# Optimization experiments

Hardware: AMD Instinct MI355X
Metric: run time of the kernel (lower is better)

The kernel has to match this reference:

```python
import jax, jax.numpy as jnp
import numpy as np

KSIZE, H, W = 11, 256, 256
IN_C, OUT_C, B = 3, 64, 4


def _foveated_coords(height, width, k):
    """Integer foveated sampling coords [H, W, k, k] for y and x.

    Ring scale per kernel tap: Chebyshev dist from center -> 1/3/5/7.
    Matches FoveatedSamplingConv2d._create_all_foveated_kernels, where
    coords are exact integers, so bilinear grid_sample == integer gather.
    """
    c = k // 2
    ki = np.arange(k)
    dist = np.maximum(np.abs(ki[:, None] - c), np.abs(ki[None, :] - c))  # [k,k]
    scale = np.where(dist <= 1, 1, np.where(dist == 2, 3, np.where(dist == 3, 5, 7)))
    off_y = (ki[:, None] - c) * scale  # [k,k]
    off_x = (ki[None, :] - c) * scale  # [k,k]
    yy = np.arange(height)[:, None, None, None]
    xx = np.arange(width)[None, :, None, None]
    sy = np.clip(yy + off_y[None, None], 0, height - 1)  # [H,W,k,k]
    sx = np.clip(xx + off_x[None, None], 0, width - 1)   # [H,W,k,k]
    return jnp.asarray(sy, jnp.int32), jnp.asarray(sx, jnp.int32)


def setup_inputs() -> dict:
    key = jax.random.key(0)
    k1, k2, k3 = jax.random.split(key, 3)
    x = jax.random.normal(k1, (B, IN_C, H, W), dtype=jnp.float32)
    # Kaiming-uniform-ish init scale (exact distribution irrelevant for correctness)
    fan_in = IN_C * KSIZE * KSIZE
    bound = 1.0 / np.sqrt(fan_in)
    weight = jax.random.uniform(k2, (OUT_C, IN_C, KSIZE, KSIZE), dtype=jnp.float32,
                                minval=-bound, maxval=bound)
    bias = jax.random.uniform(k3, (OUT_C,), dtype=jnp.float32, minval=-bound, maxval=bound)
    sy, sx = _foveated_coords(H, W, KSIZE)
    return {"x": x, "weight": weight, "bias": bias, "sy": sy, "sx": sx}


def reference(x, weight, bias, sy, sx):
    # Irregular gather: sampled[b,c,h,w,ki,kj] = x[b,c, sy[h,w,ki,kj], sx[h,w,ki,kj]]
    sampled = x[:, :, sy, sx]  # [B, C, H, W, k, k]
    out = jnp.einsum('bchwkl,ockl->bohw', sampled, weight)
    return out + bias[None, :, None, None]
```

## Files before the change

### kernel.cpp

```cpp
#include <hip/hip_runtime.h>


#define HH 256
#define WW 256
#define INC 3
#define OC 64
#define KS 11
#define BB 4
#define NKC 12
#define PH 326
#define PW 512
#define PAD 35
#define NPAR 4
#define HALFR 163

typedef __attribute__((ext_vector_type(4))) float f32x4;
typedef __attribute__((ext_vector_type(8))) short s16x8;
typedef unsigned int u32;
typedef unsigned short u16;

static __device__ __forceinline__ u16 f2bf(float f) {
    u32 u = __builtin_bit_cast(u32, f);
    u32 r = (u + 0x7FFFu + ((u >> 16) & 1u)) >> 16;
    return (u16)r;
}

__global__ void __launch_bounds__(256)
prep_fused(const float* __restrict__ x, const float* __restrict__ w,
           u16* __restrict__ xs, u16* __restrict__ wf) {
    const int tid = threadIdx.x;
    if (blockIdx.x < 96) {
        int i = blockIdx.x * 256 + tid;
        int j    = i & 7;
        int lane = (i >> 3) & 63;
        int ot   = (i >> 9) & 3;
        int kc   = i >> 11;
        int o  = ot * 16 + (lane & 15);
        int k  = kc * 32 + ((lane >> 4) << 3) + j;
        int c  = k >> 7;
        int tt = k & 127;
        float val = 0.f;
        if (tt < 121) {
            int ky = tt / 11, kx = tt % 11;
            val = w[((o * INC + c) * KS + ky) * KS + kx];
        }
        wf[i] = f2bf(val);
    } else {
        const int pb = blockIdx.x - 96;
        const int k  = pb & 7;
        const int i  = pb >> 3;
        const int r  = i * 2 + (tid >> 7);
        const int zl = r / HALFR;
        const int pz = r - zl * HALFR;
        const int b    = k >> 1;
        const int py   = (k & 1) * HALFR + pz;
        const int c    = zl % INC;
        const int par  = zl / INC;
        const int z    = (b * NPAR + par) * INC + c;
        const int px0  = (tid & 127) * 4;
        const int sy   = min(max(py - PAD, 0), HH - 1);
        const float* src = x + (((size_t)b * INC + c) * HH + sy) * WW;
        ushort4 o4;
        int s0 = min(max(px0 + 0 - PAD + par, 0), WW - 1);
        int s1 = min(max(px0 + 1 - PAD + par, 0), WW - 1);
        int s2 = min(max(px0 + 2 - PAD + par, 0), WW - 1);
        int s3 = min(max(px0 + 3 - PAD + par, 0), WW - 1);
        o4.x = f2bf(src[s0]); o4.y = f2bf(src[s1]);
        o4.z = f2bf(src[s2]); o4.w = f2bf(src[s3]);
        *(ushort4*)&xs[((size_t)z * PH + py) * PW + px0] = o4;
    }
}

__global__ void __launch_bounds__(256, 3)
fov_mfma5(const u16* __restrict__ xs, const u16* __restrict__ wf,
          const float* __restrict__ bias, float* __restrict__ out) {
    __shared__ u32 offF[NKC * 32];
    const int tid = threadIdx.x;
    for (int t = tid; t < NKC * 32; t += 256) {
        int c = t >> 7, tt = t & 127;
        int dy = 0, dx = 0;
        if (tt < 121) {
            int ky = tt / 11, kx = tt - (tt / 11) * 11;
            int ay = ky - 5, ax = kx - 5;
            int d = max(abs(ay), abs(ax));
            int sc = (d <= 1) ? 1 : (d == 2 ? 3 : (d == 3 ? 5 : 7));
            dy = ay * sc; dx = ax * sc;
        }
        int par = (PAD + dx) & 3;
        offF[t] = (u32)(((((par * INC + c) * PH) + (PAD + dy)) * PW
                         + (PAD + dx - par)) * 2);
    }
    __syncthreads();

    const int lane = tid & 63;
    const int wv   = tid >> 6;
    const int obid = (blockIdx.x & 7) * 128 + (blockIdx.x >> 3);
    const int b = obid >> 8;
    const int h = obid & 255;
    const int g16 = lane & 15;
    const int kg  = lane >> 4;

    const char* xpb = (const char*)(xs + (size_t)b * (NPAR * INC * PH * PW));
    const u32 pxoff = (u32)((h * PW + wv * 64 + 4 * g16) * 2);
    const s16x8* wbase = (const s16x8*)wf;

    f32x4 acc[4][4];
#pragma unroll
    for (int T = 0; T < 4; ++T)
#pragma unroll
        for (int ob = 0; ob < 4; ++ob) acc[T][ob] = (f32x4){0, 0, 0, 0};

    uint2 G[3][8];
    s16x8 A[2][4];

#define STAGE_G(S, KC)                                                    \
    {                                                                     \
        const uint4* fp = (const uint4*)&offF[(KC) * 32 + kg * 8];        \
        const uint4 fA = fp[0], fB = fp[1];                               \
        G[S][0] = *(const uint2*)(xpb + (pxoff + fA.x));                  \
        G[S][1] = *(const uint2*)(xpb + (pxoff + fA.y));                  \
        G[S][2] = *(const uint2*)(xpb + (pxoff + fA.z));                  \
        G[S][3] = *(const uint2*)(xpb + (pxoff + fA.w));                  \
        G[S][4] = *(const uint2*)(xpb + (pxoff + fB.x));                  \
        G[S][5] = *(const uint2*)(xpb + (pxoff + fB.y));                  \
        G[S][6] = *(const uint2*)(xpb + (pxoff + fB.z));                  \
        G[S][7] = *(const uint2*)(xpb + (pxoff + fB.w));                  \
    }

    STAGE_G(0, 0)
    STAGE_G(1, 1)
    {
        const s16x8* wp = wbase + lane;
        A[0][0] = wp[0]; A[0][1] = wp[64]; A[0][2] = wp[128]; A[0][3] = wp[192];
    }

#pragma unroll
    for (int kc = 0; kc < NKC; ++kc) {
        const int cur = kc % 3;
        const int pre = (kc + 2) % 3;
        if (kc + 2 < NKC) STAGE_G(pre, kc + 2)
        if (kc + 1 < NKC) {
            const s16x8* wp = wbase + (((kc + 1) << 8) + lane);
            A[(kc + 1) & 1][0] = wp[0];   A[(kc + 1) & 1][1] = wp[64];
            A[(kc + 1) & 1][2] = wp[128]; A[(kc + 1) & 1][3] = wp[192];
        }
        __builtin_amdgcn_s_setprio(1);
#pragma unroll
        for (int T = 0; T < 4; ++T) {
            const u32 sel = (T & 1) ? 0x07060302u : 0x05040100u;
            const bool hi = (T >> 1) != 0;
            union { u32 u[4]; s16x8 v; } bu;
            bu.u[0] = __builtin_amdgcn_perm(hi ? G[cur][1].y : G[cur][1].x,
                                            hi ? G[cur][0].y : G[cur][0].x, sel);
            bu.u[1] = __builtin_amdgcn_perm(hi ? G[cur][3].y : G[cur][3].x,
                                            hi ? G[cur][2].y : G[cur][2].x, sel);
            bu.u[2] = __builtin_amdgcn_perm(hi ? G[cur][5].y : G[cur][5].x,
                                            hi ? G[cur][4].y : G[cur][4].x, sel);
            bu.u[3] = __builtin_amdgcn_perm(hi ? G[cur][7].y : G[cur][7].x,
                                            hi ? G[cur][6].y : G[cur][6].x, sel);

            acc[T][0] = __builtin_amdgcn_mfma_f32_16x16x32_bf16(A[kc & 1][0], bu.v, acc[T][0], 0, 0, 0);
            acc[T][1] = __builtin_amdgcn_mfma_f32_16x16x32_bf16(A[kc & 1][1], bu.v, acc[T][1], 0, 0, 0);
            acc[T][2] = __builtin_amdgcn_mfma_f32_16x16x32_bf16(A[kc & 1][2], bu.v, acc[T][2], 0, 0, 0);
            acc[T][3] = __builtin_amdgcn_mfma_f32_16x16x32_bf16(A[kc & 1][3], bu.v, acc[T][3], 0, 0, 0);
        }
        __builtin_amdgcn_s_setprio(0);
    }
#undef STAGE_G

    const int orow = kg << 2;
    const float4* bp = (const float4*)bias;
#pragma unroll
    for (int ob = 0; ob < 4; ++ob) {
        const float4 bb = bp[ob * 4 + kg];
        const float bv[4] = {bb.x, bb.y, bb.z, bb.w};
#pragma unroll
        for (int r = 0; r < 4; ++r) {
            const int o = ob * 16 + orow + r;
            f32x4 st;
            st[0] = acc[0][ob][r] + bv[r];
            st[1] = acc[1][ob][r] + bv[r];
            st[2] = acc[2][ob][r] + bv[r];
            st[3] = acc[3][ob][r] + bv[r];
            float* op = out + (((size_t)b * OC + o) * HH + h) * WW + wv * 64 + 4 * g16;
            __builtin_nontemporal_store(st, (f32x4*)op);
        }
    }
}

__global__ void fovconv_transpose_w(const float* __restrict__ w,
                                    float* __restrict__ wT) {
    int i = blockIdx.x * 256 + threadIdx.x;
    const int N = OC * INC * KS * KS;
    if (i < N) {
        int o  = i / (INC * KS * KS);
        int ct = i % (INC * KS * KS);
        wT[ct * OC + o] = w[i];
    }
}

__global__ void __launch_bounds__(256)
fovconv_main(const float* __restrict__ x, const float* __restrict__ wT,
             const float* __restrict__ bias, float* __restrict__ out) {
    const int wpix = threadIdx.x;
    const int h    = blockIdx.x & (HH - 1);
    const int b    = blockIdx.x >> 8;
    float acc[OC];
#pragma unroll
    for (int o = 0; o < OC; ++o) acc[o] = 0.f;
    const float* xbp = x + (size_t)b * INC * HH * WW;
    for (int k = 0; k < KS; ++k) {
        const int dy = k - 5;
        for (int l = 0; l < KS; ++l) {
            const int dx = l - 5;
            const int d  = max(abs(dy), abs(dx));
            const int scale = (d <= 1) ? 1 : (d == 2 ? 3 : (d == 3 ? 5 : 7));
            const int sy = min(max(h + dy * scale, 0), HH - 1);
            const int sx = min(max(wpix + dx * scale, 0), WW - 1);
            const int base = sy * WW + sx;
            const int t = k * KS + l;
#pragma unroll
            for (int c = 0; c < INC; ++c) {
                const float xv = xbp[c * (HH * WW) + base];
                const float* wp = wT + (c * (KS * KS) + t) * OC;
#pragma unroll
                for (int o = 0; o < OC; ++o)
                    acc[o] = fmaf(xv, wp[o], acc[o]);
            }
        }
    }
    float* op = out + (((size_t)b * OC) * HH + h) * WW + wpix;
#pragma unroll
    for (int o = 0; o < OC; ++o)
        op[(size_t)o * HH * WW] = acc[o] + bias[o];
}

extern "C" void kernel_launch(void* const* d_in, const int* in_sizes, int n_in,
                              void* d_out, int out_size, void* d_ws, size_t ws_size,
                              hipStream_t stream) {
    const float* x    = (const float*)d_in[0];
    const float* wgt  = (const float*)d_in[1];
    const float* bias = (const float*)d_in[2];
    float* out = (float*)d_out;

    const size_t xs_bytes = (size_t)BB * NPAR * INC * PH * PW * 2;
    const size_t wf_bytes = (size_t)NKC * 4 * 64 * 8 * 2;

    if (ws_size >= xs_bytes + wf_bytes) {
        u16* xsb = (u16*)d_ws;
        u16* wf  = (u16*)((char*)d_ws + xs_bytes);
        prep_fused<<<96 + 978 * 8, 256, 0, stream>>>(x, wgt, xsb, wf);
        fov_mfma5<<<BB * HH, 256, 0, stream>>>(xsb, wf, bias, out);
    } else {
        float* wT = (float*)d_ws;
        const int NW = OC * INC * KS * KS;
        fovconv_transpose_w<<<(NW + 255) / 256, 256, 0, stream>>>(wgt, wT);
        fovconv_main<<<BB * HH, 256, 0, stream>>>(x, wT, bias, out);
    }
}
```

Before: 36.65 us.

## Stage weights into LDS via direct global-to-LDS loads, shrink gather prefetch depth

Each block now copies the full bf16 weight fragment array (48KB) into shared memory at kernel start using global_load_lds, and reads A operands from LDS every k-chunk instead of prefetching them from global memory into registers. The gather pipeline is reduced from three stages to two, freeing registers. The intent is to cut per-wave global weight traffic and register pressure. The cost is a large LDS footprint, which may limit occupancy below the 3 blocks per CU requested in the launch bounds, plus a shallower latency-hiding window for the gathers.

```diff
diff --git a/kernel.cpp b/kernel.cpp
--- a/kernel.cpp
+++ b/kernel.cpp
@@ -74,8 +74,13 @@
 __global__ void __launch_bounds__(256, 3)
 fov_mfma5(const u16* __restrict__ xs, const u16* __restrict__ wf,
           const float* __restrict__ bias, float* __restrict__ out) {
+    __shared__ __align__(16) u32 swf[NKC * 1024];
     __shared__ u32 offF[NKC * 32];
-    const int tid = threadIdx.x;
+
+    const int tid  = threadIdx.x;
+    const int lane = tid & 63;
+    const int wv   = tid >> 6;
+
     for (int t = tid; t < NKC * 32; t += 256) {
         int c = t >> 7, tt = t & 127;
         int dy = 0, dx = 0;
@@ -90,10 +95,22 @@
         offF[t] = (u32)(((((par * INC + c) * PH) + (PAD + dy)) * PW
                          + (PAD + dx - par)) * 2);
     }
+
+    {
+        const char* wsrc = (const char*)wf;
+#pragma unroll
+        for (int j = 0; j < NKC; ++j) {
+            const int chunkbase = j * 256 + wv * 64;
+            __builtin_amdgcn_global_load_lds(
+                (const __attribute__((address_space(1))) void*)
+                    (wsrc + ((size_t)(chunkbase + lane) << 4)),
+                (__attribute__((address_space(3))) void*)
+                    ((char*)swf + ((size_t)chunkbase << 4)),
+                16, 0, 0);
+        }
+    }
     __syncthreads();
 
-    const int lane = tid & 63;
-    const int wv   = tid >> 6;
     const int obid = (blockIdx.x & 7) * 128 + (blockIdx.x >> 3);
     const int b = obid >> 8;
     const int h = obid & 255;
@@ -102,7 +119,7 @@
 
     const char* xpb = (const char*)(xs + (size_t)b * (NPAR * INC * PH * PW));
     const u32 pxoff = (u32)((h * PW + wv * 64 + 4 * g16) * 2);
-    const s16x8* wbase = (const s16x8*)wf;
+    const s16x8* wlds = (const s16x8*)swf;
 
     f32x4 acc[4][4];
 #pragma unroll
@@ -110,8 +127,7 @@
 #pragma unroll
         for (int ob = 0; ob < 4; ++ob) acc[T][ob] = (f32x4){0, 0, 0, 0};
 
-    uint2 G[3][8];
-    s16x8 A[2][4];
+    uint2 G[2][8];
 
 #define STAGE_G(S, KC)                                                    \
     {                                                                     \
@@ -128,22 +144,17 @@
     }
 
     STAGE_G(0, 0)
-    STAGE_G(1, 1)
-    {
-        const s16x8* wp = wbase + lane;
-        A[0][0] = wp[0]; A[0][1] = wp[64]; A[0][2] = wp[128]; A[0][3] = wp[192];
-    }
 
 #pragma unroll
     for (int kc = 0; kc < NKC; ++kc) {
-        const int cur = kc % 3;
-        const int pre = (kc + 2) % 3;
-        if (kc + 2 < NKC) STAGE_G(pre, kc + 2)
-        if (kc + 1 < NKC) {
-            const s16x8* wp = wbase + (((kc + 1) << 8) + lane);
-            A[(kc + 1) & 1][0] = wp[0];   A[(kc + 1) & 1][1] = wp[64];
-            A[(kc + 1) & 1][2] = wp[128]; A[(kc + 1) & 1][3] = wp[192];
-        }
+        const int cur = kc & 1;
+        if (kc + 1 < NKC) STAGE_G(cur ^ 1, kc + 1)
+
+        const s16x8 a0 = wlds[(kc << 8) + lane];
+        const s16x8 a1 = wlds[(kc << 8) + 64 + lane];
+        const s16x8 a2 = wlds[(kc << 8) + 128 + lane];
+        const s16x8 a3 = wlds[(kc << 8) + 192 + lane];
+
         __builtin_amdgcn_s_setprio(1);
 #pragma unroll
         for (int T = 0; T < 4; ++T) {
@@ -159,10 +170,10 @@
             bu.u[3] = __builtin_amdgcn_perm(hi ? G[cur][7].y : G[cur][7].x,
                                             hi ? G[cur][6].y : G[cur][6].x, sel);
 
-            acc[T][0] = __builtin_amdgcn_mfma_f32_16x16x32_bf16(A[kc & 1][0], bu.v, acc[T][0], 0, 0, 0);
-            acc[T][1] = __builtin_amdgcn_mfma_f32_16x16x32_bf16(A[kc & 1][1], bu.v, acc[T][1], 0, 0, 0);
-            acc[T][2] = __builtin_amdgcn_mfma_f32_16x16x32_bf16(A[kc & 1][2], bu.v, acc[T][2], 0, 0, 0);
-            acc[T][3] = __builtin_amdgcn_mfma_f32_16x16x32_bf16(A[kc & 1][3], bu.v, acc[T][3], 0, 0, 0);
+            acc[T][0] = __builtin_amdgcn_mfma_f32_16x16x32_bf16(a0, bu.v, acc[T][0], 0, 0, 0);
+            acc[T][1] = __builtin_amdgcn_mfma_f32_16x16x32_bf16(a1, bu.v, acc[T][1], 0, 0, 0);
+            acc[T][2] = __builtin_amdgcn_mfma_f32_16x16x32_bf16(a2, bu.v, acc[T][2], 0, 0, 0);
+            acc[T][3] = __builtin_amdgcn_mfma_f32_16x16x32_bf16(a3, bu.v, acc[T][3], 0, 0, 0);
         }
         __builtin_amdgcn_s_setprio(0);
     }
```

Measured after the change: 33.04 us (median of 3 runs). 9.8% less time.
